# Kernel optimization log

Hardware: AMD Instinct MI355X
Metric: run time of the kernel (lower is better)

Reference implementation:

```python
import jax, jax.numpy as jnp
import numpy as np

B, S, D, H, F = 4, 2048, 1024, 16, 2048
DK = D // H
EPS = 1e-5


def layernorm(x, g, b):
    mu = jnp.mean(x, axis=-1, keepdims=True)
    var = jnp.mean(jnp.square(x - mu), axis=-1, keepdims=True)
    return (x - mu) * jax.lax.rsqrt(var + EPS) * g + b


def setup_inputs() -> dict:
    key = jax.random.key(0)
    ks = jax.random.split(key, 16)
    s = 0.02
    inp = {
        "src_representations_batch": jax.random.normal(ks[0], (B, S, D), jnp.float32),
        "src_mask": jnp.ones((B, 1, 1, S), dtype=bool),
        "wq": jax.random.normal(ks[1], (D, D), jnp.float32) * s,
        "bq": jnp.zeros((D,), jnp.float32),
        "wk": jax.random.normal(ks[2], (D, D), jnp.float32) * s,
        "bk": jnp.zeros((D,), jnp.float32),
        "wv": jax.random.normal(ks[3], (D, D), jnp.float32) * s,
        "bv": jnp.zeros((D,), jnp.float32),
        "wo": jax.random.normal(ks[4], (D, D), jnp.float32) * s,
        "bo": jnp.zeros((D,), jnp.float32),
        "ln1_g": jnp.ones((D,), jnp.float32),
        "ln1_b": jnp.zeros((D,), jnp.float32),
        "ln2_g": jnp.ones((D,), jnp.float32),
        "ln2_b": jnp.zeros((D,), jnp.float32),
        "w1": jax.random.normal(ks[5], (D, F), jnp.float32) * s,
        "b1": jnp.zeros((F,), jnp.float32),
        "w2": jax.random.normal(ks[6], (F, D), jnp.float32) * s,
        "b2": jnp.zeros((D,), jnp.float32),
    }
    return inp


def reference(src_representations_batch, src_mask, wq, bq, wk, bk, wv, bv, wo, bo,
              ln1_g, ln1_b, ln2_g, ln2_b, w1, b1, w2, b2):
    x = src_representations_batch
    # sublayer 1: x + MHA(LN(x))   (dropout is identity at inference)
    h = layernorm(x, ln1_g, ln1_b)  # [B,S,D]
    q = (h @ wq + bq).reshape(B, S, H, DK).transpose(0, 2, 1, 3)  # [B,H,S,DK]
    k = (h @ wk + bk).reshape(B, S, H, DK).transpose(0, 2, 1, 3)
    v = (h @ wv + bv).reshape(B, S, H, DK).transpose(0, 2, 1, 3)
    scores = jnp.einsum("bhqd,bhkd->bhqk", q, k) / jnp.sqrt(jnp.float32(DK))
    scores = jnp.where(src_mask, scores, jnp.float32(-jnp.inf))
    attn = jax.nn.softmax(scores, axis=-1)
    ctx = jnp.einsum("bhqk,bhkd->bhqd", attn, v)  # [B,H,S,DK]
    ctx = ctx.transpose(0, 2, 1, 3).reshape(B, S, D)
    x = x + (ctx @ wo + bo)
    # sublayer 2: x + FFN(LN(x))
    h2 = layernorm(x, ln2_g, ln2_b)
    ff = jax.nn.relu(h2 @ w1 + b1) @ w2 + b2
    return x + ff
```

## Files before the change

kernel.cpp:

```cpp
#include <hip/hip_runtime.h>
#include <hip/hip_bf16.h>
#include <cstdint>
#include <cstddef>

typedef __attribute__((ext_vector_type(8))) __bf16 bf16x8;
typedef __attribute__((ext_vector_type(4))) __bf16 bf16x4;
typedef __attribute__((ext_vector_type(4))) float f32x4;
typedef __attribute__((ext_vector_type(16))) float f32x16;

constexpr int SEQ = 2048, DIM = 1024, NB = 4, NH = 16, HD = 64, FFD = 2048;
constexpr int MR = NB * SEQ;
constexpr int QKVN = 3 * DIM;
constexpr int QKN = 2 * DIM;
#define QSCALE 0.18033688011112042f

#define AS1 __attribute__((address_space(1)))
#define AS3 __attribute__((address_space(3)))

__device__ __forceinline__ void gload_lds16(const void* g, void* l) {
  __builtin_amdgcn_global_load_lds((const AS1 void*)g, (AS3 void*)l, 16, 0, 0);
}

__device__ __forceinline__ float exp2x(float x) {
#if __has_builtin(__builtin_amdgcn_exp2f)
  return __builtin_amdgcn_exp2f(x);
#else
  return exp2f(x);
#endif
}

__device__ __forceinline__ uint32_t cvtpk(float lo, float hi) {
  uint32_t r;
  asm("v_cvt_pk_bf16_f32 %0, %1, %2" : "=v"(r) : "v"(lo), "v"(hi));
  return r;
}

__device__ __forceinline__ void pl32swap(uint32_t& a, uint32_t& b) {
  asm volatile("v_permlane32_swap_b32 %0, %1" : "+v"(a), "+v"(b));
}

__device__ __forceinline__ void memfence() { asm volatile("" ::: "memory"); }

__global__ __launch_bounds__(256) void transpose_all(const float* __restrict__ wq,
                                                     const float* __restrict__ wk,
                                                     const float* __restrict__ wv,
                                                     const float* __restrict__ wo,
                                                     const float* __restrict__ w1,
                                                     const float* __restrict__ w2,
                                                     __bf16* __restrict__ wqkvt,
                                                     __bf16* __restrict__ wot,
                                                     __bf16* __restrict__ w1t,
                                                     __bf16* __restrict__ w2t) {
  const int id = blockIdx.x;
  const float* W;
  __bf16* Wt;
  int K, N, local;
  float scale = 1.0f;
  if (id < 3072) {
    K = DIM; N = DIM;
    local = id & 1023;
    if (id < 1024)      { W = wq; Wt = wqkvt;                        scale = QSCALE; }
    else if (id < 2048) { W = wk; Wt = wqkvt + (size_t)DIM * DIM; }
    else                { W = wv; Wt = wqkvt + (size_t)2 * DIM * DIM; }
  } else if (id < 4096) {
    W = wo; Wt = wot; K = DIM; N = DIM; local = id - 3072;
  } else if (id < 6144) {
    W = w1; Wt = w1t; K = DIM; N = FFD; local = id - 4096;
  } else {
    W = w2; Wt = w2t; K = FFD; N = DIM; local = id - 6144;
  }
  const int ntn = N >> 5;
  const int bn = (local % ntn) * 32, bk = (local / ntn) * 32;

  __shared__ float tile[32][33];
  const int t = threadIdx.x;
  const int r = t >> 5, c = t & 31;
#pragma unroll
  for (int p = 0; p < 4; ++p)
    tile[r + p * 8][c] = W[(size_t)(bk + r + p * 8) * N + bn + c];
  __syncthreads();
#pragma unroll
  for (int p = 0; p < 4; ++p)
    Wt[(size_t)(bn + r + p * 8) * K + bk + c] = (__bf16)(tile[c][r + p * 8] * scale);
}

__global__ __launch_bounds__(256) void bias_fuse(const float* __restrict__ bq,
                                                 const float* __restrict__ bk,
                                                 const float* __restrict__ bv,
                                                 float* __restrict__ o) {
  const int i = blockIdx.x * 256 + threadIdx.x;
  o[i] = (i < DIM) ? bq[i] * QSCALE : (i < 2 * DIM ? bk[i - DIM] : bv[i - 2 * DIM]);
}

__global__ __launch_bounds__(256) void ln_kernel(const float* __restrict__ x,
                                                 const float* __restrict__ g,
                                                 const float* __restrict__ b,
                                                 __bf16* __restrict__ out) {
  const int row = blockIdx.x;
  const int t = threadIdx.x;
  const float4 v = ((const float4*)(x + (size_t)row * DIM))[t];
  float s = v.x + v.y + v.z + v.w;
  float ss = v.x * v.x + v.y * v.y + v.z * v.z + v.w * v.w;
#pragma unroll
  for (int off = 32; off; off >>= 1) {
    s += __shfl_down(s, off);
    ss += __shfl_down(ss, off);
  }
  __shared__ float red[10];
  const int wave = t >> 6, lane = t & 63;
  if (lane == 0) { red[wave] = s; red[4 + wave] = ss; }
  __syncthreads();
  if (t == 0) {
    float S = red[0] + red[1] + red[2] + red[3];
    float SS = red[4] + red[5] + red[6] + red[7];
    float mu = S * (1.0f / DIM);
    float var = SS * (1.0f / DIM) - mu * mu;
    red[8] = mu;
    red[9] = rsqrtf(var + 1e-5f);
  }
  __syncthreads();
  const float mu = red[8], ri = red[9];
  const float4 gv = ((const float4*)g)[t];
  const float4 bv = ((const float4*)b)[t];
  bf16x4 o;
  o[0] = (__bf16)((v.x - mu) * ri * gv.x + bv.x);
  o[1] = (__bf16)((v.y - mu) * ri * gv.y + bv.y);
  o[2] = (__bf16)((v.z - mu) * ri * gv.z + bv.z);
  o[3] = (__bf16)((v.w - mu) * ri * gv.w + bv.w);
  *(bf16x4*)(out + (size_t)row * DIM + t * 4) = o;
}

template <bool RELU, bool ADD_RES, bool OUT_BF16, bool VOUT>
__global__ __launch_bounds__(512, 2) void gemm256(const __bf16* __restrict__ A,
                                                  const __bf16* __restrict__ Bt,
                                                  const float* __restrict__ bias,
                                                  const float* __restrict__ resid,
                                                  void* __restrict__ Cout,
                                                  __bf16* __restrict__ Vt,
                                                  int M, int N, int K, int ldc,
                                                  float bscale) {
  __shared__ __bf16 lds[2][32768];
  const int t = threadIdx.x;
  const int wave = t >> 6, lane = t & 63;
  const int lr = lane & 15, l4 = lane >> 4;
  const int wr = wave >> 2, wc = wave & 3;
  const int gx = gridDim.x, nwg = gx * gridDim.y;
  const int hw = blockIdx.y * gx + blockIdx.x;
  const int lgid = (hw & 7) * (nwg >> 3) + (hw >> 3);
  const int m0 = (lgid / gx) * 256, n0 = (lgid % gx) * 256;
  const int NKT = K >> 6;

  auto stage = [&](int kt, int buf) {
    const int k0 = kt << 6;
    __bf16* base = lds[buf];
#pragma unroll
    for (int j = 0; j < 4; ++j) {
      const int c = j * 512 + t;
      const int row = c >> 3, cc = (c & 7) ^ (row & 7);
      gload_lds16(A + (size_t)(m0 + row) * K + k0 + cc * 8,
                  base + (size_t)(j * 512 + wave * 64) * 8);
      gload_lds16(Bt + (size_t)(n0 + row) * K + k0 + cc * 8,
                  base + 16384 + (size_t)(j * 512 + wave * 64) * 8);
    }
  };

  stage(0, 0);
  asm volatile("s_waitcnt vmcnt(0)" ::: "memory");
  __builtin_amdgcn_s_barrier();
  memfence();

  f32x4 acc[8][4] = {};

  int cur = 0;
  for (int kt = 0; kt < NKT; ++kt) {
    if (kt + 1 < NKT) stage(kt + 1, cur ^ 1);
    const __bf16* bb = lds[cur];
    bf16x8 bf[4][2];
#pragma unroll
    for (int nj = 0; nj < 4; ++nj)
#pragma unroll
      for (int ks = 0; ks < 2; ++ks) {
        const int row = wc * 64 + nj * 16 + lr;
        bf[nj][ks] = *(const bf16x8*)(bb + 16384 + row * 64 + (((ks * 4 + l4) ^ (row & 7)) * 8));
      }
#pragma unroll
    for (int mi = 0; mi < 8; ++mi) {
      bf16x8 af[2];
#pragma unroll
      for (int ks = 0; ks < 2; ++ks) {
        const int row = wr * 128 + mi * 16 + lr;
        af[ks] = *(const bf16x8*)(bb + row * 64 + (((ks * 4 + l4) ^ (row & 7)) * 8));
      }
#pragma unroll
      for (int nj = 0; nj < 4; ++nj)
#pragma unroll
        for (int ks = 0; ks < 2; ++ks)
          acc[mi][nj] = __builtin_amdgcn_mfma_f32_16x16x32_bf16(af[ks], bf[nj][ks], acc[mi][nj], 0, 0, 0);
    }
    asm volatile("s_waitcnt vmcnt(0)" ::: "memory");
    __builtin_amdgcn_s_barrier();
    memfence();
    cur ^= 1;
  }

  const int rb0 = l4 * 4;
  if (VOUT && n0 >= 2 * DIM) {
#pragma unroll
    for (int nj = 0; nj < 4; ++nj) {
      const int colv = n0 - 2 * DIM + wc * 64 + nj * 16 + lr;
      const float bc = bias[n0 + wc * 64 + nj * 16 + lr] * bscale;
#pragma unroll
      for (int mi = 0; mi < 8; ++mi) {
        const int row = m0 + wr * 128 + mi * 16 + rb0;
        const int b = row >> 11, s = row & (SEQ - 1);
        bf16x4 o;
#pragma unroll
        for (int r = 0; r < 4; ++r) o[r] = (__bf16)(acc[mi][nj][r] + bc);
        *(bf16x4*)(Vt + ((size_t)b * NH * HD + colv) * SEQ + s) = o;
      }
    }
    return;
  }
#pragma unroll
  for (int nj = 0; nj < 4; ++nj) {
    const int col = n0 + wc * 64 + nj * 16 + lr;
    const float bc = bias[col] * bscale;
#pragma unroll
    for (int mi = 0; mi < 8; ++mi) {
#pragma unroll
      for (int r = 0; r < 4; ++r) {
        const int row = m0 + wr * 128 + mi * 16 + rb0 + r;
        float v = acc[mi][nj][r] + bc;
        if (RELU) v = fmaxf(v, 0.0f);
        if (ADD_RES) v += resid[(size_t)row * ldc + col];
        if (OUT_BF16)
          ((__bf16*)Cout)[(size_t)row * ldc + col] = (__bf16)v;
        else
          ((float*)Cout)[(size_t)row * ldc + col] = v;
      }
    }
  }
}

template <bool RELU, bool ADD_RES, bool OUT_BF16>
__global__ __launch_bounds__(512, 2) void gemm_bt(const __bf16* __restrict__ A,
                                                  const __bf16* __restrict__ Bt,
                                                  const float* __restrict__ bias,
                                                  const float* __restrict__ resid,
                                                  void* __restrict__ Cout,
                                                  int M, int N, int K, float bscale) {
  __shared__ __bf16 lds[3][24576];
  const int t = threadIdx.x;
  const int wave = t >> 6, lane = t & 63;
  const int lr = lane & 15, l4 = lane >> 4;
  const int wr = wave >> 2, wc = wave & 3;
  const int gx = gridDim.x, nwg = gx * gridDim.y;
  const int hw = blockIdx.y * gx + blockIdx.x;
  const int lgid = (hw & 7) * (nwg >> 3) + (hw >> 3);
  const int m0 = (lgid / gx) * 128, n0 = (lgid % gx) * 256;
  const int NKT = K >> 6;

  auto stage = [&](int kt, __bf16* base) {
    const int k0 = kt << 6;
    const int row = t >> 3, cc = (t & 7) ^ (row & 7);
    gload_lds16(A + (size_t)(m0 + row) * K + k0 + cc * 8,
                base + (size_t)(wave * 64) * 8);
    gload_lds16(A + (size_t)(m0 + 64 + row) * K + k0 + cc * 8,
                base + 4096 + (size_t)(wave * 64) * 8);
#pragma unroll
    for (int j = 0; j < 4; ++j) {
      const int c = j * 512 + t;
      const int br = c >> 3, bc = (c & 7) ^ (br & 7);
      gload_lds16(Bt + (size_t)(n0 + br) * K + k0 + bc * 8,
                  base + 8192 + (size_t)(j * 512 + wave * 64) * 8);
    }
  };

  __bf16* pc = lds[0];
  __bf16* pn = lds[1];
  __bf16* p2 = lds[2];

  stage(0, pc);
  stage(1, pn);
  asm volatile("s_waitcnt vmcnt(6)" ::: "memory");
  __builtin_amdgcn_s_barrier();
  memfence();

  f32x4 acc[4][4] = {};

  for (int kt = 0; kt < NKT; ++kt) {
    if (kt + 2 < NKT) stage(kt + 2, p2);

    bf16x8 af[4][2], bfr[4][2];
#pragma unroll
    for (int mi = 0; mi < 4; ++mi)
#pragma unroll
      for (int ks = 0; ks < 2; ++ks) {
        const int row = wr * 64 + mi * 16 + lr;
        af[mi][ks] = *(const bf16x8*)(pc + row * 64 + (((ks * 4 + l4) ^ (row & 7)) * 8));
      }
#pragma unroll
    for (int nj = 0; nj < 4; ++nj)
#pragma unroll
      for (int ks = 0; ks < 2; ++ks) {
        const int row = wc * 64 + nj * 16 + lr;
        bfr[nj][ks] = *(const bf16x8*)(pc + 8192 + row * 64 + (((ks * 4 + l4) ^ (row & 7)) * 8));
      }

    __builtin_amdgcn_s_setprio(1);
#pragma unroll
    for (int mi = 0; mi < 4; ++mi)
#pragma unroll
      for (int nj = 0; nj < 4; ++nj)
#pragma unroll
        for (int ks = 0; ks < 2; ++ks)
          acc[mi][nj] = __builtin_amdgcn_mfma_f32_16x16x32_bf16(af[mi][ks], bfr[nj][ks], acc[mi][nj], 0, 0, 0);
    __builtin_amdgcn_s_setprio(0);

    if (kt + 2 < NKT) { asm volatile("s_waitcnt vmcnt(6)" ::: "memory"); }
    else              { asm volatile("s_waitcnt vmcnt(0)" ::: "memory"); }
    __builtin_amdgcn_s_barrier();
    memfence();
    __bf16* tmp = pc; pc = pn; pn = p2; p2 = tmp;
  }

  const int rb0 = l4 * 4;
#pragma unroll
  for (int nj = 0; nj < 4; ++nj) {
    const int col = n0 + wc * 64 + nj * 16 + lr;
    const float bc = bias[col] * bscale;
#pragma unroll
    for (int mi = 0; mi < 4; ++mi) {
#pragma unroll
      for (int r = 0; r < 4; ++r) {
        const int row = m0 + wr * 64 + mi * 16 + rb0 + r;
        float v = acc[mi][nj][r] + bc;
        if (RELU) v = fmaxf(v, 0.0f);
        if (ADD_RES) v += resid[(size_t)row * N + col];
        if (OUT_BF16)
          ((__bf16*)Cout)[(size_t)row * N + col] = (__bf16)v;
        else
          ((float*)Cout)[(size_t)row * N + col] = v;
      }
    }
  }
}

__global__ __launch_bounds__(256, 4) void attn_kernel(const __bf16* __restrict__ Q,
                                                      const __bf16* __restrict__ Kb,
                                                      const __bf16* __restrict__ Vt,
                                                      __bf16* __restrict__ ctx, int ld) {
  __shared__ __bf16 sK[2][64 * 64];
  __shared__ __bf16 sV[2][64 * 64];
  const int t = threadIdx.x;
  const int wave = t >> 6, lane = t & 63;
  const int l31 = lane & 31, hi = lane >> 5;
  const int swz = l31 & 7;
  const int nwg = gridDim.x;
  const int hw = blockIdx.x;
  const int lid = (hw & 7) * (nwg >> 3) + (hw >> 3);
  const int qb = lid & 15, h = (lid >> 4) & 15, b = lid >> 8;
  const size_t baseq = (size_t)b * SEQ * ld + (size_t)h * HD;
  const size_t basec = (size_t)b * SEQ * DIM + (size_t)h * HD;
  const size_t vtbase = ((size_t)b * NH + h) * (size_t)HD * SEQ;
  const int q0 = qb * 128 + wave * 32;

  bf16x8 qf[4];
#pragma unroll
  for (int ks = 0; ks < 4; ++ks)
    qf[ks] = *(const bf16x8*)(Q + baseq + (size_t)(q0 + l31) * ld + ks * 16 + hi * 8);

  bf16x8 onesf;
#pragma unroll
  for (int j = 0; j < 8; ++j) onesf[j] = (__bf16)1.0f;

  f32x16 acc[2] = {};
  f32x16 lacc = {};

  auto stage = [&](int kb, int buf) {
#pragma unroll
    for (int i = 0; i < 2; ++i) {
      const int c = i * 256 + wave * 64 + lane;
      const int kr = c >> 3, kc = (c & 7) ^ (kr & 7);
      gload_lds16(Kb + baseq + (size_t)(kb * 64 + kr) * ld + kc * 8,
                  &sK[buf][(size_t)(i * 256 + wave * 64) * 8]);
      gload_lds16(Vt + vtbase + (size_t)kr * SEQ + kb * 64 + kc * 8,
                  &sV[buf][(size_t)(i * 256 + wave * 64) * 8]);
    }
  };

  stage(0, 0);
  __syncthreads();

  constexpr int NT = SEQ / 64;
  int cur = 0;
  for (int kb = 0; kb < NT; ++kb) {
    if (kb + 1 < NT) stage(kb + 1, cur ^ 1);
    const __bf16* bK = sK[cur];
    const __bf16* bV = sV[cur];

    f32x16 sc[2] = {};
#pragma unroll
    for (int kn = 0; kn < 2; ++kn) {
#pragma unroll
      for (int ks = 0; ks < 4; ++ks) {
        const bf16x8 kf = *(const bf16x8*)(bK + (size_t)(kn * 32 + l31) * 64 +
                                           (((ks * 2 + hi) ^ swz) * 8));
        sc[kn] = __builtin_amdgcn_mfma_f32_32x32x16_bf16(kf, qf[ks], sc[kn], 0, 0, 0);
      }
    }

#pragma unroll
    for (int s = 0; s < 4; ++s) {
      const int kn = s >> 1, s1 = s & 1;
      bf16x8 vf[2];
#pragma unroll
      for (int dn = 0; dn < 2; ++dn)
        vf[dn] = *(const bf16x8*)(bV + (size_t)(dn * 32 + l31) * 64 +
                                  (((s * 2 + hi) ^ swz) * 8));
      uint32_t w0 = cvtpk(exp2x(sc[kn][8 * s1 + 0]), exp2x(sc[kn][8 * s1 + 1]));
      uint32_t w1 = cvtpk(exp2x(sc[kn][8 * s1 + 2]), exp2x(sc[kn][8 * s1 + 3]));
      uint32_t w2 = cvtpk(exp2x(sc[kn][8 * s1 + 4]), exp2x(sc[kn][8 * s1 + 5]));
      uint32_t w3 = cvtpk(exp2x(sc[kn][8 * s1 + 6]), exp2x(sc[kn][8 * s1 + 7]));
      pl32swap(w0, w2);
      pl32swap(w1, w3);
      union { uint32_t u[4]; bf16x8 v; } pa;
      pa.u[0] = w0; pa.u[1] = w1; pa.u[2] = w2; pa.u[3] = w3;
      acc[0] = __builtin_amdgcn_mfma_f32_32x32x16_bf16(pa.v, vf[0], acc[0], 0, 0, 0);
      acc[1] = __builtin_amdgcn_mfma_f32_32x32x16_bf16(pa.v, vf[1], acc[1], 0, 0, 0);
      lacc   = __builtin_amdgcn_mfma_f32_32x32x16_bf16(pa.v, onesf, lacc, 0, 0, 0);
    }
    __syncthreads();
    cur ^= 1;
  }

#pragma unroll
  for (int r = 0; r < 16; ++r) {
    const int q31 = (r & 3) + 8 * (r >> 2) + 4 * hi;
    const float ir = 1.0f / lacc[r];
    const size_t row = q0 + q31;
#pragma unroll
    for (int dn = 0; dn < 2; ++dn)
      ctx[basec + row * DIM + dn * 32 + l31] = (__bf16)(acc[dn][r] * ir);
  }
}

extern "C" void kernel_launch(void* const* d_in, const int* in_sizes, int n_in,
                              void* d_out, int out_size, void* d_ws, size_t ws_size,
                              hipStream_t stream) {
  (void)in_sizes; (void)n_in; (void)out_size; (void)ws_size;
  const float* x   = (const float*)d_in[0];
  const float* wq  = (const float*)d_in[2];
  const float* bq  = (const float*)d_in[3];
  const float* wk  = (const float*)d_in[4];
  const float* bk  = (const float*)d_in[5];
  const float* wv  = (const float*)d_in[6];
  const float* bv  = (const float*)d_in[7];
  const float* wo  = (const float*)d_in[8];
  const float* bo  = (const float*)d_in[9];
  const float* g1  = (const float*)d_in[10];
  const float* be1 = (const float*)d_in[11];
  const float* g2  = (const float*)d_in[12];
  const float* be2 = (const float*)d_in[13];
  const float* w1  = (const float*)d_in[14];
  const float* b1  = (const float*)d_in[15];
  const float* w2  = (const float*)d_in[16];
  const float* b2  = (const float*)d_in[17];
  float* out = (float*)d_out;

  char* ws = (char*)d_ws;
  size_t off = 0;
  auto alloc = [&](size_t bytes) -> char* {
    char* p = ws + off;
    off += (bytes + 255) & ~(size_t)255;
    return p;
  };
  __bf16* wqkvt = (__bf16*)alloc((size_t)QKVN * DIM * 2);
  __bf16* wot   = (__bf16*)alloc((size_t)DIM * DIM * 2);
  __bf16* w1t   = (__bf16*)alloc((size_t)DIM * FFD * 2);
  __bf16* w2t   = (__bf16*)alloc((size_t)FFD * DIM * 2);
  float*  qkvb  = (float*)alloc((size_t)QKVN * 4);
  __bf16* hbuf  = (__bf16*)alloc((size_t)MR * DIM * 2);
  __bf16* qk    = (__bf16*)alloc((size_t)MR * QKN * 2);
  __bf16* vtb   = (__bf16*)alloc((size_t)MR * DIM * 2);
  __bf16* fbuf  = (__bf16*)alloc((size_t)MR * FFD * 2);
  __bf16* ctx   = hbuf;
  __bf16* h2    = qk;
  float*  x2    = (float*)d_out;

  const dim3 blk(256);
  const dim3 gblk(512);
  transpose_all<<<dim3(8192), blk, 0, stream>>>(wq, wk, wv, wo, w1, w2,
                                                wqkvt, wot, w1t, w2t);
  bias_fuse<<<dim3(QKVN / 256), blk, 0, stream>>>(bq, bk, bv, qkvb);

  ln_kernel<<<MR, blk, 0, stream>>>(x, g1, be1, hbuf);
  gemm256<false, false, true, true><<<dim3(QKVN / 256, MR / 256), gblk, 0, stream>>>(
      hbuf, wqkvt, qkvb, nullptr, qk, vtb, MR, QKVN, DIM, QKN, 1.0f);
  attn_kernel<<<dim3(NB * NH * (SEQ / 128)), blk, 0, stream>>>(qk, qk + DIM, vtb, ctx, QKN);
  gemm_bt<false, true, false><<<dim3(DIM / 256, MR / 128), gblk, 0, stream>>>(
      ctx, wot, bo, x, x2, MR, DIM, DIM, 1.0f);

  ln_kernel<<<MR, blk, 0, stream>>>(x2, g2, be2, h2);
  gemm256<true, false, true, false><<<dim3(FFD / 256, MR / 256), gblk, 0, stream>>>(
      h2, w1t, b1, nullptr, fbuf, nullptr, MR, FFD, DIM, FFD, 1.0f);
  gemm_bt<false, true, false><<<dim3(DIM / 256, MR / 128), gblk, 0, stream>>>(
      fbuf, w2t, b2, x2, out, MR, DIM, FFD, 1.0f);
}
```

Before: 274.5 us.

## Split 256x256 GEMM tile into quadrants with interleaved staged loads and setprio

Reworks the big 256x256 GEMM main loop so each wave computes four 64x32 quadrant blocks. Per-half-tile global-to-LDS loads for the next K-step are issued between quadrant MFMA batches, with partial vmcnt waits and barriers in place of one full wait per iteration. MFMA sections are wrapped in s_setprio to favour matrix issue. The wave-to-output mapping changes, so the epilogue indexing is rewritten to match. The aim is to hide global-load latency and cut LDS register pressure, at the cost of more barriers per iteration and a risk of hazards if the vmcnt counts are wrong.

```diff
diff --git a/kernel.cpp b/kernel.cpp
--- a/kernel.cpp
+++ b/kernel.cpp
@@ -150,54 +150,101 @@
   const int m0 = (lgid / gx) * 256, n0 = (lgid % gx) * 256;
   const int NKT = K >> 6;
 
-  auto stage = [&](int kt, int buf) {
+  auto stageA = [&](int kt, int h, int buf) {
     const int k0 = kt << 6;
     __bf16* base = lds[buf];
 #pragma unroll
-    for (int j = 0; j < 4; ++j) {
+    for (int j = 2 * h; j < 2 * h + 2; ++j) {
       const int c = j * 512 + t;
       const int row = c >> 3, cc = (c & 7) ^ (row & 7);
       gload_lds16(A + (size_t)(m0 + row) * K + k0 + cc * 8,
                   base + (size_t)(j * 512 + wave * 64) * 8);
+    }
+  };
+  auto stageB = [&](int kt, int h, int buf) {
+    const int k0 = kt << 6;
+    __bf16* base = lds[buf];
+#pragma unroll
+    for (int j = 2 * h; j < 2 * h + 2; ++j) {
+      const int c = j * 512 + t;
+      const int row = c >> 3, cc = (c & 7) ^ (row & 7);
       gload_lds16(Bt + (size_t)(n0 + row) * K + k0 + cc * 8,
                   base + 16384 + (size_t)(j * 512 + wave * 64) * 8);
     }
   };
 
-  stage(0, 0);
-  asm volatile("s_waitcnt vmcnt(0)" ::: "memory");
+  f32x4 acc[8][4] = {};
+  bf16x8 af[4][2], bf0[2][2], bf1[2][2];
+  const __bf16* bb = lds[0];
+
+  auto rdA = [&](int ah) {
+#pragma unroll
+    for (int mi = 0; mi < 4; ++mi)
+#pragma unroll
+      for (int ks = 0; ks < 2; ++ks) {
+        const int row = ah * 128 + wr * 64 + mi * 16 + lr;
+        af[mi][ks] = *(const bf16x8*)(bb + row * 64 + (((ks * 4 + l4) ^ (row & 7)) * 8));
+      }
+  };
+  auto rdB = [&](int bh, bf16x8 (&bfr)[2][2]) {
+#pragma unroll
+    for (int nj = 0; nj < 2; ++nj)
+#pragma unroll
+      for (int ks = 0; ks < 2; ++ks) {
+        const int row = bh * 128 + wc * 32 + nj * 16 + lr;
+        bfr[nj][ks] = *(const bf16x8*)(bb + 16384 + row * 64 + (((ks * 4 + l4) ^ (row & 7)) * 8));
+      }
+  };
+  auto mm = [&](int ah, int bh, bf16x8 (&bfr)[2][2]) {
+#pragma unroll
+    for (int mi = 0; mi < 4; ++mi)
+#pragma unroll
+      for (int nj = 0; nj < 2; ++nj)
+#pragma unroll
+        for (int ks = 0; ks < 2; ++ks)
+          acc[ah * 4 + mi][bh * 2 + nj] = __builtin_amdgcn_mfma_f32_16x16x32_bf16(
+              af[mi][ks], bfr[nj][ks], acc[ah * 4 + mi][bh * 2 + nj], 0, 0, 0);
+  };
+
+  stageA(0, 0, 0); stageB(0, 0, 0); stageB(0, 1, 0); stageA(0, 1, 0);
+  asm volatile("s_waitcnt vmcnt(4)" ::: "memory");
   __builtin_amdgcn_s_barrier();
   memfence();
 
-  f32x4 acc[8][4] = {};
-
   int cur = 0;
   for (int kt = 0; kt < NKT; ++kt) {
-    if (kt + 1 < NKT) stage(kt + 1, cur ^ 1);
-    const __bf16* bb = lds[cur];
-    bf16x8 bf[4][2];
-#pragma unroll
-    for (int nj = 0; nj < 4; ++nj)
-#pragma unroll
-      for (int ks = 0; ks < 2; ++ks) {
-        const int row = wc * 64 + nj * 16 + lr;
-        bf[nj][ks] = *(const bf16x8*)(bb + 16384 + row * 64 + (((ks * 4 + l4) ^ (row & 7)) * 8));
-      }
-#pragma unroll
-    for (int mi = 0; mi < 8; ++mi) {
-      bf16x8 af[2];
-#pragma unroll
-      for (int ks = 0; ks < 2; ++ks) {
-        const int row = wr * 128 + mi * 16 + lr;
-        af[ks] = *(const bf16x8*)(bb + row * 64 + (((ks * 4 + l4) ^ (row & 7)) * 8));
-      }
-#pragma unroll
-      for (int nj = 0; nj < 4; ++nj)
-#pragma unroll
-        for (int ks = 0; ks < 2; ++ks)
-          acc[mi][nj] = __builtin_amdgcn_mfma_f32_16x16x32_bf16(af[ks], bf[nj][ks], acc[mi][nj], 0, 0, 0);
-    }
-    asm volatile("s_waitcnt vmcnt(0)" ::: "memory");
+    bb = lds[cur];
+    const bool pf = (kt + 1 < NKT);
+    const int nb = cur ^ 1;
+    rdA(0); rdB(0, bf0);
+    if (pf) stageA(kt + 1, 0, nb);
+    __builtin_amdgcn_s_setprio(1);
+    mm(0, 0, bf0);
+    __builtin_amdgcn_s_setprio(0);
+    if (pf) { asm volatile("s_waitcnt vmcnt(4)" ::: "memory"); }
+    else    { asm volatile("s_waitcnt vmcnt(0)" ::: "memory"); }
+    __builtin_amdgcn_s_barrier();
+    memfence();
+    rdB(1, bf1);
+    if (pf) stageB(kt + 1, 0, nb);
+    __builtin_amdgcn_s_setprio(1);
+    mm(0, 1, bf1);
+    __builtin_amdgcn_s_setprio(0);
+    if (pf) { asm volatile("s_waitcnt vmcnt(4)" ::: "memory"); }
+    else    { asm volatile("s_waitcnt vmcnt(0)" ::: "memory"); }
+    __builtin_amdgcn_s_barrier();
+    memfence();
+    rdA(1);
+    if (pf) stageB(kt + 1, 1, nb);
+    __builtin_amdgcn_s_setprio(1);
+    mm(1, 1, bf1);
+    __builtin_amdgcn_s_setprio(0);
+    if (pf) stageA(kt + 1, 1, nb);
+    __builtin_amdgcn_s_setprio(1);
+    mm(1, 0, bf0);
+    __builtin_amdgcn_s_setprio(0);
+    if (pf) { asm volatile("s_waitcnt vmcnt(4)" ::: "memory"); }
+    else    { asm volatile("s_waitcnt vmcnt(0)" ::: "memory"); }
     __builtin_amdgcn_s_barrier();
     memfence();
     cur ^= 1;
@@ -206,31 +253,32 @@
   const int rb0 = l4 * 4;
   if (VOUT && n0 >= 2 * DIM) {
 #pragma unroll
-    for (int nj = 0; nj < 4; ++nj) {
-      const int colv = n0 - 2 * DIM + wc * 64 + nj * 16 + lr;
-      const float bc = bias[n0 + wc * 64 + nj * 16 + lr] * bscale;
-#pragma unroll
-      for (int mi = 0; mi < 8; ++mi) {
-        const int row = m0 + wr * 128 + mi * 16 + rb0;
+    for (int nj4 = 0; nj4 < 4; ++nj4) {
+      const int gnc = (nj4 >> 1) * 128 + wc * 32 + (nj4 & 1) * 16 + lr;
+      const int colv = n0 - 2 * DIM + gnc;
+      const float bc = bias[n0 + gnc] * bscale;
+#pragma unroll
+      for (int mi8 = 0; mi8 < 8; ++mi8) {
+        const int row = m0 + (mi8 >> 2) * 128 + wr * 64 + (mi8 & 3) * 16 + rb0;
         const int b = row >> 11, s = row & (SEQ - 1);
         bf16x4 o;
 #pragma unroll
-        for (int r = 0; r < 4; ++r) o[r] = (__bf16)(acc[mi][nj][r] + bc);
+        for (int r = 0; r < 4; ++r) o[r] = (__bf16)(acc[mi8][nj4][r] + bc);
         *(bf16x4*)(Vt + ((size_t)b * NH * HD + colv) * SEQ + s) = o;
       }
     }
     return;
   }
 #pragma unroll
-  for (int nj = 0; nj < 4; ++nj) {
-    const int col = n0 + wc * 64 + nj * 16 + lr;
+  for (int nj4 = 0; nj4 < 4; ++nj4) {
+    const int col = n0 + (nj4 >> 1) * 128 + wc * 32 + (nj4 & 1) * 16 + lr;
     const float bc = bias[col] * bscale;
 #pragma unroll
-    for (int mi = 0; mi < 8; ++mi) {
+    for (int mi8 = 0; mi8 < 8; ++mi8) {
 #pragma unroll
       for (int r = 0; r < 4; ++r) {
-        const int row = m0 + wr * 128 + mi * 16 + rb0 + r;
-        float v = acc[mi][nj][r] + bc;
+        const int row = m0 + (mi8 >> 2) * 128 + wr * 64 + (mi8 & 3) * 16 + rb0 + r;
+        float v = acc[mi8][nj4][r] + bc;
         if (RELU) v = fmaxf(v, 0.0f);
         if (ADD_RES) v += resid[(size_t)row * ldc + col];
         if (OUT_BF16)
```

Measured after the change: 274.5 us. About the same (+0.0%).

## Replace both GEMM kernels with a single 128x128 tile, triple-buffered, BK=32 GEMM

Applied to the files above, without the earlier changes.

Replaces the 256x256 double-buffered GEMM and the 128x256 triple-buffered GEMM with one kernel that uses 128x128 output tiles, 256 threads, a K step of 32 and three LDS buffers. All four projection/FFN GEMMs now launch this kernel with more, smaller workgroups. The aim is higher occupancy and a deeper prefetch pipeline. In exchange, each K step does less reuse per byte loaded and issues more barriers, and the setprio hint from the old kernel is dropped.

```diff
diff --git a/kernel.cpp b/kernel.cpp
--- a/kernel.cpp
+++ b/kernel.cpp
@@ -131,7 +131,7 @@
 }
 
 template <bool RELU, bool ADD_RES, bool OUT_BF16, bool VOUT>
-__global__ __launch_bounds__(512, 2) void gemm256(const __bf16* __restrict__ A,
+__global__ __launch_bounds__(256, 3) void gemm128(const __bf16* __restrict__ A,
                                                   const __bf16* __restrict__ Bt,
                                                   const float* __restrict__ bias,
                                                   const float* __restrict__ resid,
@@ -139,79 +139,79 @@
                                                   __bf16* __restrict__ Vt,
                                                   int M, int N, int K, int ldc,
                                                   float bscale) {
-  __shared__ __bf16 lds[2][32768];
+  __shared__ __bf16 lds[3][8192];
   const int t = threadIdx.x;
   const int wave = t >> 6, lane = t & 63;
   const int lr = lane & 15, l4 = lane >> 4;
-  const int wr = wave >> 2, wc = wave & 3;
+  const int wr = wave >> 1, wc = wave & 1;
   const int gx = gridDim.x, nwg = gx * gridDim.y;
   const int hw = blockIdx.y * gx + blockIdx.x;
   const int lgid = (hw & 7) * (nwg >> 3) + (hw >> 3);
-  const int m0 = (lgid / gx) * 256, n0 = (lgid % gx) * 256;
-  const int NKT = K >> 6;
-
-  auto stage = [&](int kt, int buf) {
-    const int k0 = kt << 6;
-    __bf16* base = lds[buf];
-#pragma unroll
-    for (int j = 0; j < 4; ++j) {
-      const int c = j * 512 + t;
-      const int row = c >> 3, cc = (c & 7) ^ (row & 7);
+  const int m0 = (lgid / gx) * 128, n0 = (lgid % gx) * 128;
+  const int NKT = K >> 5;
+
+  auto stage = [&](int kt, __bf16* base) {
+    const int k0 = kt << 5;
+#pragma unroll
+    for (int j = 0; j < 2; ++j) {
+      const int c = j * 256 + t;
+      const int row = c >> 2, cc = (c & 3) ^ (row & 3);
       gload_lds16(A + (size_t)(m0 + row) * K + k0 + cc * 8,
-                  base + (size_t)(j * 512 + wave * 64) * 8);
+                  base + (size_t)(j * 256 + wave * 64) * 8);
       gload_lds16(Bt + (size_t)(n0 + row) * K + k0 + cc * 8,
-                  base + 16384 + (size_t)(j * 512 + wave * 64) * 8);
+                  base + 4096 + (size_t)(j * 256 + wave * 64) * 8);
     }
   };
 
-  stage(0, 0);
-  asm volatile("s_waitcnt vmcnt(0)" ::: "memory");
+  __bf16* pc = lds[0];
+  __bf16* pn = lds[1];
+  __bf16* p2 = lds[2];
+
+  stage(0, pc);
+  stage(1, pn);
+  asm volatile("s_waitcnt vmcnt(4)" ::: "memory");
   __builtin_amdgcn_s_barrier();
   memfence();
 
-  f32x4 acc[8][4] = {};
-
-  int cur = 0;
+  f32x4 acc[4][4] = {};
+
   for (int kt = 0; kt < NKT; ++kt) {
-    if (kt + 1 < NKT) stage(kt + 1, cur ^ 1);
-    const __bf16* bb = lds[cur];
-    bf16x8 bf[4][2];
-#pragma unroll
-    for (int nj = 0; nj < 4; ++nj)
-#pragma unroll
-      for (int ks = 0; ks < 2; ++ks) {
-        const int row = wc * 64 + nj * 16 + lr;
-        bf[nj][ks] = *(const bf16x8*)(bb + 16384 + row * 64 + (((ks * 4 + l4) ^ (row & 7)) * 8));
-      }
-#pragma unroll
-    for (int mi = 0; mi < 8; ++mi) {
-      bf16x8 af[2];
-#pragma unroll
-      for (int ks = 0; ks < 2; ++ks) {
-        const int row = wr * 128 + mi * 16 + lr;
-        af[ks] = *(const bf16x8*)(bb + row * 64 + (((ks * 4 + l4) ^ (row & 7)) * 8));
-      }
+    if (kt + 2 < NKT) stage(kt + 2, p2);
+
+    bf16x8 af[4], bfr[4];
+#pragma unroll
+    for (int mi = 0; mi < 4; ++mi) {
+      const int row = wr * 64 + mi * 16 + lr;
+      af[mi] = *(const bf16x8*)(pc + row * 32 + ((l4 ^ (row & 3)) * 8));
+    }
+#pragma unroll
+    for (int nj = 0; nj < 4; ++nj) {
+      const int row = wc * 64 + nj * 16 + lr;
+      bfr[nj] = *(const bf16x8*)(pc + 4096 + row * 32 + ((l4 ^ (row & 3)) * 8));
+    }
+#pragma unroll
+    for (int mi = 0; mi < 4; ++mi)
 #pragma unroll
       for (int nj = 0; nj < 4; ++nj)
-#pragma unroll
-        for (int ks = 0; ks < 2; ++ks)
-          acc[mi][nj] = __builtin_amdgcn_mfma_f32_16x16x32_bf16(af[ks], bf[nj][ks], acc[mi][nj], 0, 0, 0);
-    }
-    asm volatile("s_waitcnt vmcnt(0)" ::: "memory");
+        acc[mi][nj] = __builtin_amdgcn_mfma_f32_16x16x32_bf16(af[mi], bfr[nj], acc[mi][nj], 0, 0, 0);
+
+    if (kt + 2 < NKT) { asm volatile("s_waitcnt vmcnt(4)" ::: "memory"); }
+    else              { asm volatile("s_waitcnt vmcnt(0)" ::: "memory"); }
     __builtin_amdgcn_s_barrier();
     memfence();
-    cur ^= 1;
+    __bf16* tmp = pc; pc = pn; pn = p2; p2 = tmp;
   }
 
   const int rb0 = l4 * 4;
   if (VOUT && n0 >= 2 * DIM) {
 #pragma unroll
     for (int nj = 0; nj < 4; ++nj) {
-      const int colv = n0 - 2 * DIM + wc * 64 + nj * 16 + lr;
-      const float bc = bias[n0 + wc * 64 + nj * 16 + lr] * bscale;
-#pragma unroll
-      for (int mi = 0; mi < 8; ++mi) {
-        const int row = m0 + wr * 128 + mi * 16 + rb0;
+      const int gnc = wc * 64 + nj * 16 + lr;
+      const int colv = n0 - 2 * DIM + gnc;
+      const float bc = bias[n0 + gnc] * bscale;
+#pragma unroll
+      for (int mi = 0; mi < 4; ++mi) {
+        const int row = m0 + wr * 64 + mi * 16 + rb0;
         const int b = row >> 11, s = row & (SEQ - 1);
         bf16x4 o;
 #pragma unroll
@@ -226,10 +226,10 @@
     const int col = n0 + wc * 64 + nj * 16 + lr;
     const float bc = bias[col] * bscale;
 #pragma unroll
-    for (int mi = 0; mi < 8; ++mi) {
+    for (int mi = 0; mi < 4; ++mi) {
 #pragma unroll
       for (int r = 0; r < 4; ++r) {
-        const int row = m0 + wr * 128 + mi * 16 + rb0 + r;
+        const int row = m0 + wr * 64 + mi * 16 + rb0 + r;
         float v = acc[mi][nj][r] + bc;
         if (RELU) v = fmaxf(v, 0.0f);
         if (ADD_RES) v += resid[(size_t)row * ldc + col];
@@ -237,110 +237,6 @@
           ((__bf16*)Cout)[(size_t)row * ldc + col] = (__bf16)v;
         else
           ((float*)Cout)[(size_t)row * ldc + col] = v;
-      }
-    }
-  }
-}
-
-template <bool RELU, bool ADD_RES, bool OUT_BF16>
-__global__ __launch_bounds__(512, 2) void gemm_bt(const __bf16* __restrict__ A,
-                                                  const __bf16* __restrict__ Bt,
-                                                  const float* __restrict__ bias,
-                                                  const float* __restrict__ resid,
-                                                  void* __restrict__ Cout,
-                                                  int M, int N, int K, float bscale) {
-  __shared__ __bf16 lds[3][24576];
-  const int t = threadIdx.x;
-  const int wave = t >> 6, lane = t & 63;
-  const int lr = lane & 15, l4 = lane >> 4;
-  const int wr = wave >> 2, wc = wave & 3;
-  const int gx = gridDim.x, nwg = gx * gridDim.y;
-  const int hw = blockIdx.y * gx + blockIdx.x;
-  const int lgid = (hw & 7) * (nwg >> 3) + (hw >> 3);
-  const int m0 = (lgid / gx) * 128, n0 = (lgid % gx) * 256;
-  const int NKT = K >> 6;
-
-  auto stage = [&](int kt, __bf16* base) {
-    const int k0 = kt << 6;
-    const int row = t >> 3, cc = (t & 7) ^ (row & 7);
-    gload_lds16(A + (size_t)(m0 + row) * K + k0 + cc * 8,
-                base + (size_t)(wave * 64) * 8);
-    gload_lds16(A + (size_t)(m0 + 64 + row) * K + k0 + cc * 8,
-                base + 4096 + (size_t)(wave * 64) * 8);
-#pragma unroll
-    for (int j = 0; j < 4; ++j) {
-      const int c = j * 512 + t;
-      const int br = c >> 3, bc = (c & 7) ^ (br & 7);
-      gload_lds16(Bt + (size_t)(n0 + br) * K + k0 + bc * 8,
-                  base + 8192 + (size_t)(j * 512 + wave * 64) * 8);
-    }
-  };
-
-  __bf16* pc = lds[0];
-  __bf16* pn = lds[1];
-  __bf16* p2 = lds[2];
-
-  stage(0, pc);
-  stage(1, pn);
-  asm volatile("s_waitcnt vmcnt(6)" ::: "memory");
-  __builtin_amdgcn_s_barrier();
-  memfence();
-
-  f32x4 acc[4][4] = {};
-
-  for (int kt = 0; kt < NKT; ++kt) {
-    if (kt + 2 < NKT) stage(kt + 2, p2);
-
-    bf16x8 af[4][2], bfr[4][2];
-#pragma unroll
-    for (int mi = 0; mi < 4; ++mi)
-#pragma unroll
-      for (int ks = 0; ks < 2; ++ks) {
-        const int row = wr * 64 + mi * 16 + lr;
-        af[mi][ks] = *(const bf16x8*)(pc + row * 64 + (((ks * 4 + l4) ^ (row & 7)) * 8));
-      }
-#pragma unroll
-    for (int nj = 0; nj < 4; ++nj)
-#pragma unroll
-      for (int ks = 0; ks < 2; ++ks) {
-        const int row = wc * 64 + nj * 16 + lr;
-        bfr[nj][ks] = *(const bf16x8*)(pc + 8192 + row * 64 + (((ks * 4 + l4) ^ (row & 7)) * 8));
-      }
-
-    __builtin_amdgcn_s_setprio(1);
-#pragma unroll
-    for (int mi = 0; mi < 4; ++mi)
-#pragma unroll
-      for (int nj = 0; nj < 4; ++nj)
-#pragma unroll
-        for (int ks = 0; ks < 2; ++ks)
-          acc[mi][nj] = __builtin_amdgcn_mfma_f32_16x16x32_bf16(af[mi][ks], bfr[nj][ks], acc[mi][nj], 0, 0, 0);
-    __builtin_amdgcn_s_setprio(0);
-
-    if (kt + 2 < NKT) { asm volatile("s_waitcnt vmcnt(6)" ::: "memory"); }
-    else              { asm volatile("s_waitcnt vmcnt(0)" ::: "memory"); }
-    __builtin_amdgcn_s_barrier();
-    memfence();
-    __bf16* tmp = pc; pc = pn; pn = p2; p2 = tmp;
-  }
-
-  const int rb0 = l4 * 4;
-#pragma unroll
-  for (int nj = 0; nj < 4; ++nj) {
-    const int col = n0 + wc * 64 + nj * 16 + lr;
-    const float bc = bias[col] * bscale;
-#pragma unroll
-    for (int mi = 0; mi < 4; ++mi) {
-#pragma unroll
-      for (int r = 0; r < 4; ++r) {
-        const int row = m0 + wr * 64 + mi * 16 + rb0 + r;
-        float v = acc[mi][nj][r] + bc;
-        if (RELU) v = fmaxf(v, 0.0f);
-        if (ADD_RES) v += resid[(size_t)row * N + col];
-        if (OUT_BF16)
-          ((__bf16*)Cout)[(size_t)row * N + col] = (__bf16)v;
-        else
-          ((float*)Cout)[(size_t)row * N + col] = v;
       }
     }
   }
@@ -489,21 +385,20 @@
   float*  x2    = (float*)d_out;
 
   const dim3 blk(256);
-  const dim3 gblk(512);
   transpose_all<<<dim3(8192), blk, 0, stream>>>(wq, wk, wv, wo, w1, w2,
                                                 wqkvt, wot, w1t, w2t);
   bias_fuse<<<dim3(QKVN / 256), blk, 0, stream>>>(bq, bk, bv, qkvb);
 
   ln_kernel<<<MR, blk, 0, stream>>>(x, g1, be1, hbuf);
-  gemm256<false, false, true, true><<<dim3(QKVN / 256, MR / 256), gblk, 0, stream>>>(
+  gemm128<false, false, true, true><<<dim3(QKVN / 128, MR / 128), blk, 0, stream>>>(
       hbuf, wqkvt, qkvb, nullptr, qk, vtb, MR, QKVN, DIM, QKN, 1.0f);
   attn_kernel<<<dim3(NB * NH * (SEQ / 128)), blk, 0, stream>>>(qk, qk + DIM, vtb, ctx, QKN);
-  gemm_bt<false, true, false><<<dim3(DIM / 256, MR / 128), gblk, 0, stream>>>(
-      ctx, wot, bo, x, x2, MR, DIM, DIM, 1.0f);
+  gemm128<false, true, false, false><<<dim3(DIM / 128, MR / 128), blk, 0, stream>>>(
+      ctx, wot, bo, x, x2, nullptr, MR, DIM, DIM, DIM, 1.0f);
 
   ln_kernel<<<MR, blk, 0, stream>>>(x2, g2, be2, h2);
-  gemm256<true, false, true, false><<<dim3(FFD / 256, MR / 256), gblk, 0, stream>>>(
+  gemm128<true, false, true, false><<<dim3(FFD / 128, MR / 128), blk, 0, stream>>>(
       h2, w1t, b1, nullptr, fbuf, nullptr, MR, FFD, DIM, FFD, 1.0f);
-  gemm_bt<false, true, false><<<dim3(DIM / 256, MR / 128), gblk, 0, stream>>>(
-      fbuf, w2t, b2, x2, out, MR, DIM, FFD, 1.0f);
-}
+  gemm128<false, true, false, false><<<dim3(DIM / 128, MR / 128), blk, 0, stream>>>(
+      fbuf, w2t, b2, x2, out, nullptr, MR, DIM, FFD, DIM, 1.0f);
+}
```

New measurement: 294.1 us. 7.2% more time.
